# Kernel optimization log

Measured on AMD Instinct MI355X. Metric: run time of the kernel, lower is better.

The kernel has to match this reference:

```python
import jax, jax.numpy as jnp
import numpy as np
import math

B, S, D, H = 4, 512, 768, 12
HD = D // H  # 64
NREL = 2 * 50 + 1  # 101


def setup_inputs() -> dict:
    key = jax.random.key(0)
    ks = jax.random.split(key, 16)
    sc = 0.02
    inp = {
        "query": jax.random.normal(ks[0], (B, S, D), jnp.float32),
        "key": jax.random.normal(ks[1], (B, S, D), jnp.float32),
        "value": jax.random.normal(ks[2], (B, S, D), jnp.float32),
        "mask": jax.random.randint(ks[3], (B, S), 0, 2, jnp.int32),
        "graph_arc": jax.random.randint(ks[4], (B, S, S), 0, NREL, jnp.int64),
        "Wq": jax.random.normal(ks[5], (D, D), jnp.float32) * sc,
        "bq": jnp.zeros((D,), jnp.float32),
        "Wk": jax.random.normal(ks[6], (D, D), jnp.float32) * sc,
        "bk": jnp.zeros((D,), jnp.float32),
        "Wv": jax.random.normal(ks[7], (D, D), jnp.float32) * sc,
        "bv": jnp.zeros((D,), jnp.float32),
        "Wo": jax.random.normal(ks[8], (D, D), jnp.float32) * sc,
        "bo": jnp.zeros((D,), jnp.float32),
        "Ek": jax.random.normal(ks[9], (NREL, HD), jnp.float32) * sc,  # dp_relation_k_g
        "Eq": jax.random.normal(ks[10], (NREL, HD), jnp.float32) * sc,  # dp_relation_q_g
        "Ev": jax.random.normal(ks[11], (NREL, HD), jnp.float32) * sc,  # dp_relation_v_g
    }
    return inp


def _shape(x):
    # (b, s, d) -> (b, h, s, hd)
    return x.reshape(B, S, H, HD).transpose(0, 2, 1, 3)


def reference(query, key, value, mask, graph_arc, Wq, bq, Wk, bk, Wv, bv, Wo, bo, Ek, Eq, Ev):
    q = _shape(query @ Wq.T + bq)   # (b, h, s, hd)
    k = _shape(key @ Wk.T + bk)
    v = _shape(value @ Wv.T + bv)

    scores = jnp.einsum('bhqe,bhke->bhqk', q, k)  # raw QK^T

    dp_k = Ek[graph_arc]  # (b, s, r, hd) relation key embeddings
    dp_q = Eq[graph_arc]  # (b, s, r, hd) relation query embeddings (use_two_attn)
    dp_v = Ev[graph_arc]  # (b, s, r, hd) relation value embeddings (not just_attn)

    key_dp = jnp.einsum('bhse,bsre->bhsr', q, dp_k)
    query_dp = jnp.einsum('bhse,bsre->bhsr', k, dp_q)
    scores = (scores + query_dp + key_dp) / math.sqrt(HD)

    neg_inf = jnp.float32(-jnp.inf)
    maskb = (mask == 0)[:, None, None, :]  # (b, 1, 1, k)
    scores = jnp.where(maskb, neg_inf, scores)
    weights = jax.nn.softmax(scores, axis=-1)  # (b, h, s, r)

    context = jnp.einsum('bhqk,bhke->bhqe', weights, v)
    # relative_matmul_dpv: (b,h,s,r) x (b,s,r,e) -> (b,h,s,e)
    context = context + jnp.einsum('bhsr,bsre->bhse', weights, dp_v)

    context = context.transpose(0, 2, 1, 3).reshape(B, S, D)  # unshape
    out = context @ Wo.T + bo
    return out
```

## Files before the change

### kernel.cpp

```cpp
#include <hip/hip_runtime.h>
#include <hip/hip_bf16.h>
#include <cfloat>
#include <cstdint>

#define Bb 4
#define Ss 512
#define Dd 768
#define Hh 12
#define HDd 64
#define NREL 101

typedef __attribute__((ext_vector_type(8))) short bfrag;
typedef __attribute__((ext_vector_type(4))) float f32x4;
typedef __attribute__((ext_vector_type(8))) unsigned short u16x8;

static __device__ __forceinline__ unsigned short f2bf(float x) {
  union { __hip_bfloat16 h; unsigned short u; } c;
  c.h = __float2bfloat16(x);
  return c.u;
}
static __device__ __forceinline__ float bf2f(unsigned short u) {
  return __uint_as_float(((unsigned int)u) << 16);
}
static __device__ __forceinline__ f32x4 mfma3(bfrag a, bfrag b, f32x4 c) {
  return __builtin_amdgcn_mfma_f32_16x16x32_bf16(a, b, c, 0, 0, 0);
}
static __device__ __forceinline__ void gload16(const void* g, void* l) {
  __builtin_amdgcn_global_load_lds((const __attribute__((address_space(1))) void*)g,
                                   (__attribute__((address_space(3))) void*)l, 16, 0, 0);
}

__global__ void detect_kernel(const int* __restrict__ g, int* __restrict__ flag) {
  __shared__ int anynz;
  if (threadIdx.x == 0) anynz = 0;
  __syncthreads();
  int acc = 0;
  for (int i = threadIdx.x; i < 4096; i += 256) acc |= g[2 * i + 1];
  if (acc != 0) atomicOr(&anynz, 1);
  __syncthreads();
  if (threadIdx.x == 0) *flag = (anynz == 0) ? 1 : 0;
}

__global__ __launch_bounds__(256) void relcvt_kernel(const int* __restrict__ g,
                                                     const int* __restrict__ flag,
                                                     unsigned char* __restrict__ rel8) {
  const int idx = blockIdx.x * 256 + threadIdx.x;
  uchar4 o;
  if (*flag) {
    const int4* p = (const int4*)g + (size_t)idx * 2;
    int4 a = p[0], b = p[1];
    o = make_uchar4((unsigned char)a.x, (unsigned char)a.z,
                    (unsigned char)b.x, (unsigned char)b.z);
  } else {
    int4 a = ((const int4*)g)[idx];
    o = make_uchar4((unsigned char)a.x, (unsigned char)a.y,
                    (unsigned char)a.z, (unsigned char)a.w);
  }
  ((uchar4*)rel8)[idx] = o;
}

__global__ __launch_bounds__(256) void ecvt_kernel(
    const float* __restrict__ Ek, const float* __restrict__ Eq, const float* __restrict__ Ev,
    unsigned short* __restrict__ ekH, unsigned short* __restrict__ ekL,
    unsigned short* __restrict__ eqH, unsigned short* __restrict__ eqL,
    unsigned short* __restrict__ evtH, unsigned short* __restrict__ evtL)
{
  const int i = blockIdx.x * 256 + threadIdx.x;
  if (i < 896) {
    const int row = i >> 3, s8 = i & 7;
    u16x8 H1, L1, H2, L2;
#pragma unroll
    for (int j = 0; j < 8; j++) {
      const float a = (row < NREL) ? Ek[row * 64 + s8 * 8 + j] : 0.f;
      const float b = (row < NREL) ? Eq[row * 64 + s8 * 8 + j] : 0.f;
      unsigned short h1 = f2bf(a); H1[j] = h1; L1[j] = f2bf(a - bf2f(h1));
      unsigned short h2 = f2bf(b); H2[j] = h2; L2[j] = f2bf(b - bf2f(h2));
    }
    const size_t dst = (size_t)row * 64 + (size_t)((s8 ^ (row & 7)) << 3);
    *(u16x8*)&ekH[dst] = H1; *(u16x8*)&ekL[dst] = L1;
    *(u16x8*)&eqH[dst] = H2; *(u16x8*)&eqL[dst] = L2;
  }
  if (i < 1024) {
    const int d = i >> 4, s8 = i & 15;
    const int c = s8 >> 3, sl = s8 & 7;
    u16x8 H, L;
#pragma unroll
    for (int j = 0; j < 8; j++) {
      const int g = c * 64 + sl * 8 + j;
      const float v = (g < NREL) ? Ev[g * 64 + d] : 0.f;
      unsigned short h = f2bf(v); H[j] = h; L[j] = f2bf(v - bf2f(h));
    }
    const size_t dst = (size_t)d * 128 + c * 64 + (size_t)((sl ^ (d & 7)) << 3);
    *(u16x8*)&evtH[dst] = H; *(u16x8*)&evtL[dst] = L;
  }
}

struct CvtJob { const float* src; unsigned short* hi; unsigned short* lo; int rowlen; int nslots; };
struct Cvt8 { CvtJob j[8]; };

__global__ __launch_bounds__(256) void convert_kernel(Cvt8 jobs) {
  CvtJob jb = jobs.j[blockIdx.z];
  int idx = blockIdx.x * 256 + threadIdx.x;
  if (idx >= jb.nslots) return;
  const int spr = jb.rowlen >> 3;
  const int row = idx / spr;
  const int srem = idx - row * spr;
  const int c = srem >> 3, s8 = srem & 7;
  const float4* s4 = (const float4*)(jb.src + (size_t)idx * 8);
  float4 v0 = s4[0], v1 = s4[1];
  float e[8] = {v0.x, v0.y, v0.z, v0.w, v1.x, v1.y, v1.z, v1.w};
  u16x8 H, L;
#pragma unroll
  for (int i = 0; i < 8; i++) {
    unsigned short h = f2bf(e[i]);
    H[i] = h;
    L[i] = f2bf(e[i] - bf2f(h));
  }
  size_t dst = (size_t)row * jb.rowlen + c * 64 + (size_t)((s8 ^ (row & 7)) * 8);
  *(u16x8*)(jb.hi + dst) = H;
  *(u16x8*)(jb.lo + dst) = L;
}

__global__ __launch_bounds__(256, 2) void gemm_mfma(
    const unsigned short* __restrict__ Xh0, const unsigned short* __restrict__ Xl0,
    const unsigned short* __restrict__ Xh1, const unsigned short* __restrict__ Xl1,
    const unsigned short* __restrict__ Xh2, const unsigned short* __restrict__ Xl2,
    const unsigned short* __restrict__ Wh0, const unsigned short* __restrict__ Wl0,
    const unsigned short* __restrict__ Wh1, const unsigned short* __restrict__ Wl1,
    const unsigned short* __restrict__ Wh2, const unsigned short* __restrict__ Wl2,
    const float* __restrict__ b0, const float* __restrict__ b1, const float* __restrict__ b2,
    float* __restrict__ Yf,
    unsigned short* __restrict__ oH0, unsigned short* __restrict__ oL0,
    unsigned short* __restrict__ oH1, unsigned short* __restrict__ oL1,
    unsigned short* __restrict__ oH2, unsigned short* __restrict__ oL2,
    int mode)
{
  __shared__ __align__(16) unsigned short Ah[128 * 64], Al[128 * 64];
  __shared__ __align__(16) unsigned short Bh[128 * 64], Bl[128 * 64];

  const int t = threadIdx.x;
  const int lane = t & 63, w = t >> 6;
  const int lg = lane >> 4, lc = lane & 15;
  const int wr = w >> 1, wc = w & 1;
  const int m0 = blockIdx.y * 128, n0 = blockIdx.x * 128;
  const int z = blockIdx.z;
  const unsigned short* Xh = (z == 0) ? Xh0 : (z == 1) ? Xh1 : Xh2;
  const unsigned short* Xl = (z == 0) ? Xl0 : (z == 1) ? Xl1 : Xl2;
  const unsigned short* Wh = (z == 0) ? Wh0 : (z == 1) ? Wh1 : Wh2;
  const unsigned short* Wl = (z == 0) ? Wl0 : (z == 1) ? Wl1 : Wl2;
  const float* bias = (z == 0) ? b0 : (z == 1) ? b1 : b2;

  f32x4 acc[4][4];
#pragma unroll
  for (int m = 0; m < 4; m++)
#pragma unroll
    for (int n = 0; n < 4; n++) acc[m][n] = (f32x4){0.f, 0.f, 0.f, 0.f};

  const int srow = t >> 3;
  const int scol = (t & 7) * 8;

  for (int c = 0; c < 12; c++) {
#pragma unroll
    for (int i = 0; i < 4; i++) {
      size_t ga = (size_t)(m0 + i * 32 + srow) * Dd + c * 64 + scol;
      size_t gb = (size_t)(n0 + i * 32 + srow) * Dd + c * 64 + scol;
      gload16(Xh + ga, &Ah[i * 2048 + t * 8]);
      gload16(Xl + ga, &Al[i * 2048 + t * 8]);
      gload16(Wh + gb, &Bh[i * 2048 + t * 8]);
      gload16(Wl + gb, &Bl[i * 2048 + t * 8]);
    }
    __syncthreads();
#pragma unroll
    for (int ks = 0; ks < 2; ks++) {
      bfrag ah[4], al[4];
#pragma unroll
      for (int m = 0; m < 4; m++) {
        const int aidx = (wr * 64 + m * 16 + lc) * 64 + (((ks * 4 + lg) ^ (lc & 7)) * 8);
        ah[m] = *(const bfrag*)&Ah[aidx];
        al[m] = *(const bfrag*)&Al[aidx];
      }
#pragma unroll
      for (int n = 0; n < 4; n++) {
        const int bidx = (wc * 64 + n * 16 + lc) * 64 + (((ks * 4 + lg) ^ (lc & 7)) * 8);
        bfrag bh = *(const bfrag*)&Bh[bidx];
        bfrag bl = *(const bfrag*)&Bl[bidx];
#pragma unroll
        for (int m = 0; m < 4; m++) {
          acc[m][n] = mfma3(ah[m], bh, acc[m][n]);
          acc[m][n] = mfma3(ah[m], bl, acc[m][n]);
          acc[m][n] = mfma3(al[m], bh, acc[m][n]);
        }
      }
    }
    __syncthreads();
  }

  if (mode == 1) {
#pragma unroll
    for (int n = 0; n < 4; n++) {
      const int col = n0 + wc * 64 + n * 16 + lc;
      const float badd = bias[col];
#pragma unroll
      for (int m = 0; m < 4; m++) {
        const int rbase = m0 + wr * 64 + m * 16 + 4 * lg;
#pragma unroll
        for (int i = 0; i < 4; i++)
          Yf[(size_t)(rbase + i) * Dd + col] = acc[m][n][i] + badd;
      }
    }
  } else {
    unsigned short* dH = (z == 0) ? oH0 : (z == 1) ? oH1 : oH2;
    unsigned short* dL = (z == 0) ? oL0 : (z == 1) ? oL1 : oL2;
#pragma unroll
    for (int n = 0; n < 4; n++) {
      const int col = n0 + wc * 64 + n * 16 + lc;
      const int h = col >> 6, d = col & 63;
      const float badd = bias[col];
#pragma unroll
      for (int m = 0; m < 4; m++) {
        const int rbase = m0 + wr * 64 + m * 16 + 4 * lg;
#pragma unroll
        for (int i = 0; i < 4; i++) {
          const int row = rbase + i;
          const int b = row >> 9, s = row & 511;
          const float val = acc[m][n][i] + badd;
          const unsigned short hh = f2bf(val);
          const unsigned short ll = f2bf(val - bf2f(hh));
          size_t pos;
          if (z < 2) {
            const size_t R = ((size_t)b * Hh + h) * Ss + s;
            pos = (R << 6) + (size_t)((((d >> 3) ^ (s & 7)) << 3) + (d & 7));
          } else {
            const size_t R = ((size_t)b * Hh + h) * (size_t)HDd + d;
            pos = R * Ss + (size_t)((s >> 6) << 6) +
                  (size_t)(((((s & 63) >> 3) ^ (d & 7)) << 3) + (s & 7));
          }
          dH[pos] = hh;
          dL[pos] = ll;
        }
      }
    }
  }
}

__global__ __launch_bounds__(256, 3) void attn_kernel(
    const unsigned short* __restrict__ qHg, const unsigned short* __restrict__ qLg,
    const unsigned short* __restrict__ kHg, const unsigned short* __restrict__ kLg,
    const unsigned short* __restrict__ vtHg, const unsigned short* __restrict__ vtLg,
    const unsigned short* __restrict__ ekH, const unsigned short* __restrict__ ekL,
    const unsigned short* __restrict__ eqH, const unsigned short* __restrict__ eqL,
    const unsigned short* __restrict__ evtH, const unsigned short* __restrict__ evtL,
    const int* __restrict__ msk, const unsigned char* __restrict__ rel8,
    unsigned short* __restrict__ ctxH, unsigned short* __restrict__ ctxL)
{
  __shared__ __align__(16) unsigned short table[2][16 * 112];
  __shared__ __align__(16) float wsum[2][16 * 112];
  __shared__ __align__(16) unsigned short pbuf[2][2][16 * 32];
  __shared__ __align__(16) float osum[2][64 * 16];
  __shared__ __align__(16) unsigned short wsumBF[2][16 * 128];
  __shared__ __align__(16) float l_t[2][16];

  const int t = threadIdx.x;
  const int lane = t & 63, w = t >> 6;
  const int lg = lane >> 4, lc = lane & 15;
  const int tile = w >> 1, half = w & 1;
  const int h = blockIdx.y, b = blockIdx.z;
  const int q0 = (blockIdx.x * 2 + tile) * 16;
  const size_t bh = (size_t)b * Hh + h;

  for (int i = t; i < 2 * 16 * 112; i += 256) ((float*)wsum)[i] = 0.f;
  if (t < 32) ((float*)l_t)[t] = 0.f;

  bfrag qh[2], ql[2];
  {
    const size_t roff = (bh * Ss + q0 + lc) << 6;
    bfrag kqh[2], kql[2];
#pragma unroll
    for (int es = 0; es < 2; es++) {
      const int sw = ((es * 4 + lg) ^ (lc & 7)) * 8;
      qh[es] = *(const bfrag*)&qHg[roff + sw];
      ql[es] = *(const bfrag*)&qLg[roff + sw];
      kqh[es] = *(const bfrag*)&kHg[roff + sw];
      kql[es] = *(const bfrag*)&kLg[roff + sw];
    }
    const int rc0 = half ? 4 : 0, rc1 = half ? 7 : 4;
    for (int rc = rc0; rc < rc1; rc++) {
      f32x4 acc = {0.f, 0.f, 0.f, 0.f};
      const size_t eoff = (size_t)(rc * 16 + lc) << 6;
#pragma unroll
      for (int es = 0; es < 2; es++) {
        const int sw = ((es * 4 + lg) ^ (lc & 7)) * 8;
        bfrag a1 = *(const bfrag*)&ekH[eoff + sw];
        bfrag a2 = *(const bfrag*)&ekL[eoff + sw];
        bfrag a3 = *(const bfrag*)&eqH[eoff + sw];
        bfrag a4 = *(const bfrag*)&eqL[eoff + sw];
        acc = mfma3(a1, qh[es], acc);
        acc = mfma3(a1, ql[es], acc);
        acc = mfma3(a2, qh[es], acc);
        acc = mfma3(a3, kqh[es], acc);
        acc = mfma3(a3, kql[es], acc);
        acc = mfma3(a4, kqh[es], acc);
      }
#pragma unroll
      for (int i = 0; i < 4; i++)
        table[tile][lc * 112 + rc * 16 + 4 * lg + i] = f2bf(acc[i]);
    }
  }
  __syncthreads();

  f32x4 oacc[4];
#pragma unroll
  for (int d = 0; d < 4; d++) oacc[d] = (f32x4){0.f, 0.f, 0.f, 0.f};
  float lsum = 0.f;
  const int* mrow = msk + b * Ss;
  const unsigned char* relrow = rel8 + ((size_t)b * Ss + q0 + lc) * Ss;
  unsigned short* pb = &pbuf[tile][half][0];
  const unsigned short* tab = &table[tile][lc * 112];
  float* ws_row = &wsum[tile][lc * 112];

  const int kvb = half * 256;
  const size_t kbase = (bh * Ss + kvb + lc) << 6;
  const int sw0 = (lg ^ (lc & 7)) * 8;
  const int sw1 = ((4 + lg) ^ (lc & 7)) * 8;

  bfrag c_kh[2][2], c_kl[2][2];
#pragma unroll
  for (int blk = 0; blk < 2; blk++) {
    const size_t ko = kbase + (size_t)(blk * 16) * 64;
    c_kh[blk][0] = *(const bfrag*)&kHg[ko + sw0];
    c_kh[blk][1] = *(const bfrag*)&kHg[ko + sw1];
    c_kl[blk][0] = *(const bfrag*)&kLg[ko + sw0];
    c_kl[blk][1] = *(const bfrag*)&kLg[ko + sw1];
  }

  for (int win = 0; win < 8; win++) {
    const int kv0 = kvb + win * 32;
    bfrag vh[4], vl[4];
    {
      const int col = kv0 + 8 * lg;
      const int cchunk = col >> 6, slot = (col & 63) >> 3;
#pragma unroll
      for (int dblk = 0; dblk < 4; dblk++) {
        const int drow = dblk * 16 + lc;
        const size_t va = (bh * (size_t)HDd + drow) * Ss +
                          (size_t)(cchunk << 6) + (size_t)((slot ^ (drow & 7)) << 3);
        vh[dblk] = *(const bfrag*)&vtHg[va];
        vl[dblk] = *(const bfrag*)&vtLg[va];
      }
    }
    bfrag n_kh[2][2], n_kl[2][2];
    if (win < 7) {
      const size_t kb2 = kbase + (size_t)((win + 1) * 32) * 64;
#pragma unroll
      for (int blk = 0; blk < 2; blk++) {
        const size_t ko = kb2 + (size_t)(blk * 16) * 64;
        n_kh[blk][0] = *(const bfrag*)&kHg[ko + sw0];
        n_kh[blk][1] = *(const bfrag*)&kHg[ko + sw1];
        n_kl[blk][0] = *(const bfrag*)&kLg[ko + sw0];
        n_kl[blk][1] = *(const bfrag*)&kLg[ko + sw1];
      }
    }
    f32x4 acc0 = {0.f, 0.f, 0.f, 0.f}, acc1 = {0.f, 0.f, 0.f, 0.f};
#pragma unroll
    for (int es = 0; es < 2; es++) {
      acc0 = mfma3(c_kh[0][es], qh[es], acc0);
      acc0 = mfma3(c_kh[0][es], ql[es], acc0);
      acc0 = mfma3(c_kl[0][es], qh[es], acc0);
      acc1 = mfma3(c_kh[1][es], qh[es], acc1);
      acc1 = mfma3(c_kh[1][es], ql[es], acc1);
      acc1 = mfma3(c_kl[1][es], qh[es], acc1);
    }
#pragma unroll
    for (int blk = 0; blk < 2; blk++) {
      const f32x4 a = blk ? acc1 : acc0;
      float wv[4];
#pragma unroll
      for (int i = 0; i < 4; i++) {
        const int kv = kv0 + blk * 16 + 4 * lg + i;
        const int g = relrow[kv];
        const float s = (a[i] + bf2f(tab[g])) * 0.125f;
        const float e = __expf(s);
        wv[i] = (mrow[kv] != 0) ? e : 0.f;
        lsum += wv[i];
        if (wv[i] > 0.f) atomicAdd(&ws_row[g], wv[i]);
      }
      unsigned int p01 = (unsigned int)f2bf(wv[0]) | ((unsigned int)f2bf(wv[1]) << 16);
      unsigned int p23 = (unsigned int)f2bf(wv[2]) | ((unsigned int)f2bf(wv[3]) << 16);
      *(uint2*)&pb[lc * 32 + blk * 16 + 4 * lg] = make_uint2(p01, p23);
    }
    bfrag pa = *(const bfrag*)&pb[lc * 32 + 8 * lg];
#pragma unroll
    for (int dblk = 0; dblk < 4; dblk++) {
      oacc[dblk] = mfma3(pa, vh[dblk], oacc[dblk]);
      oacc[dblk] = mfma3(pa, vl[dblk], oacc[dblk]);
    }
    if (win < 7) {
#pragma unroll
      for (int blk = 0; blk < 2; blk++)
#pragma unroll
        for (int es = 0; es < 2; es++) {
          c_kh[blk][es] = n_kh[blk][es];
          c_kl[blk][es] = n_kl[blk][es];
        }
    }
  }

  lsum += __shfl_xor(lsum, 16);
  lsum += __shfl_xor(lsum, 32);
  if (lg == 0) atomicAdd(&l_t[tile][lc], lsum);

  if (half == 0) {
#pragma unroll
    for (int dblk = 0; dblk < 4; dblk++)
      *(f32x4*)&osum[tile][lane * 16 + dblk * 4] = oacc[dblk];
  }
  __syncthreads();
  if (half == 0) return;

#pragma unroll
  for (int dblk = 0; dblk < 4; dblk++)
    oacc[dblk] += *(const f32x4*)&osum[tile][lane * 16 + dblk * 4];

  {
    const int qq = lane >> 2, seg = lane & 3;
#pragma unroll
    for (int jp = 0; jp < 16; jp++) {
      const int col = seg * 32 + jp * 2;
      const float v0 = (col < 112) ? wsum[tile][qq * 112 + col] : 0.f;
      const float v1 = (col + 1 < 112) ? wsum[tile][qq * 112 + col + 1] : 0.f;
      *(unsigned int*)&wsumBF[tile][qq * 128 + col] =
          (unsigned int)f2bf(v0) | ((unsigned int)f2bf(v1) << 16);
    }
  }

  f32x4 evacc[4];
#pragma unroll
  for (int d = 0; d < 4; d++) evacc[d] = (f32x4){0.f, 0.f, 0.f, 0.f};
#pragma unroll
  for (int es = 0; es < 4; es++) {
    bfrag pw = *(const bfrag*)&wsumBF[tile][lc * 128 + es * 32 + 8 * lg];
    const int col = es * 32 + 8 * lg;
    const int cchunk = col >> 6, slot = (col & 63) >> 3;
#pragma unroll
    for (int dblk = 0; dblk < 4; dblk++) {
      const int drow = dblk * 16 + lc;
      const size_t ea = (size_t)drow * 128 + (size_t)(cchunk << 6) +
                        (size_t)((slot ^ (drow & 7)) << 3);
      bfrag eh = *(const bfrag*)&evtH[ea];
      bfrag el = *(const bfrag*)&evtL[ea];
      evacc[dblk] = mfma3(pw, eh, evacc[dblk]);
      evacc[dblk] = mfma3(pw, el, evacc[dblk]);
    }
  }

  float rv[4];
#pragma unroll
  for (int i = 0; i < 4; i++) {
    const float lv = l_t[tile][4 * lg + i];
    rv[i] = (lv > 0.f) ? 1.f / lv : 0.f;
  }
#pragma unroll
  for (int dblk = 0; dblk < 4; dblk++) {
    const int d = dblk * 16 + lc;
    const int slot = d >> 3, pos = d & 7;
#pragma unroll
    for (int i = 0; i < 4; i++) {
      const int qrow = q0 + 4 * lg + i;
      const int r7 = qrow & 7;
      const float val = (oacc[dblk][i] + evacc[dblk][i]) * rv[i];
      const unsigned short hh = f2bf(val);
      const unsigned short ll = f2bf(val - bf2f(hh));
      const size_t base = ((size_t)b * Ss + qrow) * Dd + h * 64 +
                          (size_t)((slot ^ r7) << 3) + pos;
      ctxH[base] = hh;
      ctxL[base] = ll;
    }
  }
}

extern "C" void kernel_launch(void* const* d_in, const int* in_sizes, int n_in,
                              void* d_out, int out_size, void* d_ws, size_t ws_size,
                              hipStream_t stream) {
  const float* query = (const float*)d_in[0];
  const float* key   = (const float*)d_in[1];
  const float* value = (const float*)d_in[2];
  const int*   mask  = (const int*)d_in[3];
  const int*   garc  = (const int*)d_in[4];
  const float* Wq = (const float*)d_in[5];
  const float* bq = (const float*)d_in[6];
  const float* Wk = (const float*)d_in[7];
  const float* bk = (const float*)d_in[8];
  const float* Wv = (const float*)d_in[9];
  const float* bv = (const float*)d_in[10];
  const float* Wo = (const float*)d_in[11];
  const float* bo = (const float*)d_in[12];
  const float* Ek = (const float*)d_in[13];
  const float* Eq = (const float*)d_in[14];
  const float* Ev = (const float*)d_in[15];

  const size_t XE = (size_t)Bb * Ss * Dd;
  const size_t WE = (size_t)Dd * Dd;

  char* ws = (char*)d_ws;
  int* flag = (int*)ws;
  unsigned short* wq_h = (unsigned short*)(ws + 256);
  unsigned short* wq_l = wq_h + WE;
  unsigned short* wk_h = wq_l + WE;
  unsigned short* wk_l = wk_h + WE;
  unsigned short* wv_h = wk_l + WE;
  unsigned short* wv_l = wv_h + WE;
  unsigned short* wo_h = wv_l + WE;
  unsigned short* wo_l = wo_h + WE;
  unsigned short* xq_h = wo_l + WE;      unsigned short* xq_l = xq_h + XE;
  unsigned short* xk_h = xq_l + XE;      unsigned short* xk_l = xk_h + XE;
  unsigned short* xv_h = xk_l + XE;      unsigned short* xv_l = xv_h + XE;
  unsigned short* q_h  = xv_l + XE;      unsigned short* q_l  = q_h + XE;
  unsigned short* k_h  = q_l + XE;       unsigned short* k_l  = k_h + XE;
  unsigned short* vt_h = k_l + XE;       unsigned short* vt_l = vt_h + XE;
  unsigned short* ctx_h = vt_l + XE;     unsigned short* ctx_l = ctx_h + XE;
  unsigned char* rel8 = (unsigned char*)(ctx_l + XE);
  unsigned short* ek_h  = (unsigned short*)(rel8 + (size_t)Bb * Ss * Ss);
  unsigned short* ek_l  = ek_h + 112 * 64;
  unsigned short* eq_h  = ek_l + 112 * 64;
  unsigned short* eq_l  = eq_h + 112 * 64;
  unsigned short* evt_h = eq_l + 112 * 64;
  unsigned short* evt_l = evt_h + 64 * 128;

  detect_kernel<<<1, 256, 0, stream>>>(garc, flag);
  relcvt_kernel<<<dim3(1024), 256, 0, stream>>>(garc, flag, rel8);
  ecvt_kernel<<<dim3(4), 256, 0, stream>>>(Ek, Eq, Ev, ek_h, ek_l, eq_h, eq_l, evt_h, evt_l);

  Cvt8 pre = {};
  pre.j[0] = {query, xq_h, xq_l, Dd, (int)(XE / 8)};
  pre.j[1] = {key,   xk_h, xk_l, Dd, (int)(XE / 8)};
  pre.j[2] = {value, xv_h, xv_l, Dd, (int)(XE / 8)};
  pre.j[3] = {Wq, wq_h, wq_l, Dd, (int)(WE / 8)};
  pre.j[4] = {Wk, wk_h, wk_l, Dd, (int)(WE / 8)};
  pre.j[5] = {Wv, wv_h, wv_l, Dd, (int)(WE / 8)};
  pre.j[6] = {Wo, wo_h, wo_l, Dd, (int)(WE / 8)};
  convert_kernel<<<dim3(768, 1, 7), 256, 0, stream>>>(pre);

  gemm_mfma<<<dim3(6, 16, 3), 256, 0, stream>>>(
      xq_h, xq_l, xk_h, xk_l, xv_h, xv_l,
      wq_h, wq_l, wk_h, wk_l, wv_h, wv_l,
      bq, bk, bv, nullptr,
      q_h, q_l, k_h, k_l, vt_h, vt_l, 0);

  attn_kernel<<<dim3(16, 12, 4), 256, 0, stream>>>(
      q_h, q_l, k_h, k_l, vt_h, vt_l,
      ek_h, ek_l, eq_h, eq_l, evt_h, evt_l,
      mask, rel8, ctx_h, ctx_l);

  gemm_mfma<<<dim3(6, 16, 1), 256, 0, stream>>>(
      ctx_h, ctx_l, ctx_h, ctx_l, ctx_h, ctx_l,
      wo_h, wo_l, wo_h, wo_l, wo_h, wo_l,
      bo, bo, bo, (float*)d_out,
      nullptr, nullptr, nullptr, nullptr, nullptr, nullptr, 1);
}
```

Measured before the change: 249.8 us.

## Stage GEMM and attention epilogues through LDS for vectorized global stores

The projection GEMM epilogue now writes its bf16 hi/lo outputs into shared memory in the swizzled target layout, then each thread issues 16-byte vector stores to global memory instead of scattered 2-byte stores. The attention kernel does the same for its context output, reusing a dead LDS region. It also packs its shared buffers into one aliased array, which shrinks the LDS footprint, and raises launch bounds from 3 to 4 blocks per CU. The aim is to cut uncoalesced store traffic and raise occupancy, at the cost of an extra LDS round trip and a block barrier in the GEMM, plus tighter register limits in attention.

After: 277.8 us. 1.11x slower.

```diff
diff --git a/kernel.cpp b/kernel.cpp
--- a/kernel.cpp
+++ b/kernel.cpp
@@ -135,8 +135,11 @@
     unsigned short* __restrict__ oH2, unsigned short* __restrict__ oL2,
     int mode)
 {
-  __shared__ __align__(16) unsigned short Ah[128 * 64], Al[128 * 64];
-  __shared__ __align__(16) unsigned short Bh[128 * 64], Bl[128 * 64];
+  __shared__ __align__(16) unsigned short smem[4 * 128 * 64];
+  unsigned short* Ah = smem;
+  unsigned short* Al = smem + 8192;
+  unsigned short* Bh = smem + 16384;
+  unsigned short* Bl = smem + 24576;
 
   const int t = threadIdx.x;
   const int lane = t & 63, w = t >> 6;
@@ -211,39 +214,60 @@
   } else {
     unsigned short* dH = (z == 0) ? oH0 : (z == 1) ? oH1 : oH2;
     unsigned short* dL = (z == 0) ? oL0 : (z == 1) ? oL1 : oL2;
+    unsigned short* SH = smem;
+    unsigned short* SL = smem + 16384;
 #pragma unroll
     for (int n = 0; n < 4; n++) {
-      const int col = n0 + wc * 64 + n * 16 + lc;
-      const int h = col >> 6, d = col & 63;
-      const float badd = bias[col];
+      const int ct = wc * 64 + n * 16 + lc;
+      const float badd = bias[n0 + ct];
 #pragma unroll
       for (int m = 0; m < 4; m++) {
-        const int rbase = m0 + wr * 64 + m * 16 + 4 * lg;
 #pragma unroll
         for (int i = 0; i < 4; i++) {
-          const int row = rbase + i;
-          const int b = row >> 9, s = row & 511;
+          const int rt = wr * 64 + m * 16 + 4 * lg + i;
           const float val = acc[m][n][i] + badd;
           const unsigned short hh = f2bf(val);
           const unsigned short ll = f2bf(val - bf2f(hh));
-          size_t pos;
+          int lr, p;
           if (z < 2) {
-            const size_t R = ((size_t)b * Hh + h) * Ss + s;
-            pos = (R << 6) + (size_t)((((d >> 3) ^ (s & 7)) << 3) + (d & 7));
+            lr = rt;
+            const int d = ct & 63;
+            p = (ct & 64) + ((((d >> 3) ^ (rt & 7)) << 3) | (d & 7));
           } else {
-            const size_t R = ((size_t)b * Hh + h) * (size_t)HDd + d;
-            pos = R * Ss + (size_t)((s >> 6) << 6) +
-                  (size_t)(((((s & 63) >> 3) ^ (d & 7)) << 3) + (s & 7));
+            lr = ct;
+            p = (rt & 64) + (((((rt & 63) >> 3) ^ (ct & 7)) << 3) | (rt & 7));
           }
-          dH[pos] = hh;
-          dL[pos] = ll;
+          const int si = lr * 128 + (p ^ ((lr & 7) << 3));
+          SH[si] = hh;
+          SL[si] = ll;
         }
       }
     }
-  }
-}
-
-__global__ __launch_bounds__(256, 3) void attn_kernel(
+    __syncthreads();
+#pragma unroll
+    for (int it = 0; it < 8; it++) {
+      const int li = t * 8 + it * 2048;
+      const int lr = li >> 7, c = li & 127;
+      const int si = lr * 128 + (c ^ ((lr & 7) << 3));
+      size_t base;
+      if (z < 2) {
+        const int gr = m0 + lr;
+        const int b = gr >> 9, s = gr & 511;
+        const int h = (n0 >> 6) + (c >> 6);
+        base = ((((size_t)b * Hh + h) * Ss + s) << 6) + (c & 63);
+      } else {
+        const int b = m0 >> 9;
+        const int h = (n0 >> 6) + (lr >> 6);
+        const int d = lr & 63;
+        base = (((size_t)b * Hh + h) * (size_t)HDd + d) * Ss + (m0 & 511) + c;
+      }
+      *(u16x8*)(dH + base) = *(const u16x8*)&SH[si];
+      *(u16x8*)(dL + base) = *(const u16x8*)&SL[si];
+    }
+  }
+}
+
+__global__ __launch_bounds__(256, 4) void attn_kernel(
     const unsigned short* __restrict__ qHg, const unsigned short* __restrict__ qLg,
     const unsigned short* __restrict__ kHg, const unsigned short* __restrict__ kLg,
     const unsigned short* __restrict__ vtHg, const unsigned short* __restrict__ vtLg,
@@ -253,12 +277,13 @@
     const int* __restrict__ msk, const unsigned char* __restrict__ rel8,
     unsigned short* __restrict__ ctxH, unsigned short* __restrict__ ctxL)
 {
-  __shared__ __align__(16) unsigned short table[2][16 * 112];
-  __shared__ __align__(16) float wsum[2][16 * 112];
-  __shared__ __align__(16) unsigned short pbuf[2][2][16 * 32];
-  __shared__ __align__(16) float osum[2][64 * 16];
-  __shared__ __align__(16) unsigned short wsumBF[2][16 * 128];
-  __shared__ __align__(16) float l_t[2][16];
+  __shared__ __align__(16) char lds[33920];
+  float (*wsum)[16 * 112] = (float (*)[16 * 112])lds;
+  float (*osum)[64 * 16] = (float (*)[64 * 16])(lds + 14336);
+  unsigned short (*table)[16 * 112] = (unsigned short (*)[16 * 112])(lds + 22528);
+  unsigned short (*pbuf)[2][16 * 32] = (unsigned short (*)[2][16 * 32])(lds + 29696);
+  float* l_t = (float*)(lds + 33792);
+  unsigned short (*wsumBF)[16 * 128] = (unsigned short (*)[16 * 128])(lds + 22528);
 
   const int t = threadIdx.x;
   const int lane = t & 63, w = t >> 6;
@@ -268,8 +293,8 @@
   const int q0 = (blockIdx.x * 2 + tile) * 16;
   const size_t bh = (size_t)b * Hh + h;
 
-  for (int i = t; i < 2 * 16 * 112; i += 256) ((float*)wsum)[i] = 0.f;
-  if (t < 32) ((float*)l_t)[t] = 0.f;
+  for (int i = t; i < 2 * 16 * 112; i += 256) ((float*)lds)[i] = 0.f;
+  if (t < 32) l_t[t] = 0.f;
 
   bfrag qh[2], ql[2];
   {
@@ -314,7 +339,7 @@
   float lsum = 0.f;
   const int* mrow = msk + b * Ss;
   const unsigned char* relrow = rel8 + ((size_t)b * Ss + q0 + lc) * Ss;
-  unsigned short* pb = &pbuf[tile][half][0];
+  unsigned short* pb = pbuf[tile][half];
   const unsigned short* tab = &table[tile][lc * 112];
   float* ws_row = &wsum[tile][lc * 112];
 
@@ -407,7 +432,7 @@
 
   lsum += __shfl_xor(lsum, 16);
   lsum += __shfl_xor(lsum, 32);
-  if (lg == 0) atomicAdd(&l_t[tile][lc], lsum);
+  if (lg == 0) atomicAdd(&l_t[tile * 16 + lc], lsum);
 
   if (half == 0) {
 #pragma unroll
@@ -456,25 +481,35 @@
   float rv[4];
 #pragma unroll
   for (int i = 0; i < 4; i++) {
-    const float lv = l_t[tile][4 * lg + i];
+    const float lv = l_t[tile * 16 + 4 * lg + i];
     rv[i] = (lv > 0.f) ? 1.f / lv : 0.f;
   }
+
+  unsigned short* cH = (unsigned short*)(lds + 14336 + tile * 4096);
+  unsigned short* cL = cH + 1024;
+  asm volatile("" ::: "memory");
 #pragma unroll
   for (int dblk = 0; dblk < 4; dblk++) {
     const int d = dblk * 16 + lc;
-    const int slot = d >> 3, pos = d & 7;
 #pragma unroll
     for (int i = 0; i < 4; i++) {
-      const int qrow = q0 + 4 * lg + i;
-      const int r7 = qrow & 7;
+      const int r = 4 * lg + i;
       const float val = (oacc[dblk][i] + evacc[dblk][i]) * rv[i];
       const unsigned short hh = f2bf(val);
       const unsigned short ll = f2bf(val - bf2f(hh));
-      const size_t base = ((size_t)b * Ss + qrow) * Dd + h * 64 +
-                          (size_t)((slot ^ r7) << 3) + pos;
-      ctxH[base] = hh;
-      ctxL[base] = ll;
-    }
+      const int p = ((((d >> 3) ^ (r & 7)) << 3) | (d & 7));
+      cH[r * 64 + p] = hh;
+      cL[r * 64 + p] = ll;
+    }
+  }
+  asm volatile("" ::: "memory");
+#pragma unroll
+  for (int it = 0; it < 2; it++) {
+    const int li = lane * 8 + it * 512;
+    const int r = li >> 6, c = li & 63;
+    const size_t base = ((size_t)b * Ss + q0 + r) * Dd + h * 64 + c;
+    *(u16x8*)(ctxH + base) = *(const u16x8*)&cH[li];
+    *(u16x8*)(ctxL + base) = *(const u16x8*)&cL[li];
   }
 }
 
```
